# Performance work log

Hardware: AMD Instinct MI355X
Metric: run time of the kernel (lower is better)

Reference implementation:

```python
import jax, jax.numpy as jnp
import numpy as np
import math

GRID = 256       # grid_size
KMAX = 64        # max_elements_per_cell
RES = 512        # image resolution
SPAN = 4         # max grid cells per axis covered by one triangle bbox
NUM_VIEWS = 16
SCALE = 0.5


def _projection_matrix(x=0.5, n=1.5, f=100.0):
    return np.array([[n / x, 0.0, 0.0, 0.0],
                     [0.0, n / -x, 0.0, 0.0],
                     [0.0, 0.0, -(f + n) / (f - n), -(2.0 * f * n) / (f - n)],
                     [0.0, 0.0, -1.0, 0.0]], dtype=np.float32)


def _view_buffers(num_views, seed):
    rng = np.random.default_rng(seed)
    proj = _projection_matrix()
    mvps, lights = [], []
    for _ in range(num_views):
        u1, u2, u3 = rng.random(3)
        qx = math.sqrt(1.0 - u1) * math.sin(math.tau * u2)
        qy = math.sqrt(1.0 - u1) * math.cos(math.tau * u2)
        qz = math.sqrt(u1) * math.sin(math.tau * u3)
        qw = math.sqrt(u1) * math.cos(math.tau * u3)
        rot = np.array([[1 - 2 * (qy * qy + qz * qz), 2 * (qx * qy - qz * qw), 2 * (qx * qz + qy * qw)],
                        [2 * (qx * qy + qz * qw), 1 - 2 * (qx * qx + qz * qz), 2 * (qy * qz - qx * qw)],
                        [2 * (qx * qz - qy * qw), 2 * (qy * qz + qx * qw), 1 - 2 * (qx * qx + qy * qy)]], dtype=np.float32)
        rmat = np.eye(4, dtype=np.float32); rmat[:3, :3] = rot
        tmat = np.eye(4, dtype=np.float32); tmat[2, 3] = -4.0
        view = tmat @ rmat
        campos = np.linalg.inv(view)[:3, 3]
        light = -campos / (np.linalg.norm(campos) + 1e-8)
        mvps.append(proj @ view)
        lights.append(light.astype(np.float32))
    return np.stack(mvps).astype(np.float32), np.stack(lights).astype(np.float32)


def setup_inputs() -> dict:
    key = jax.random.key(0)
    k1, k2 = jax.random.split(key)
    F = 100_000
    # clustered per-triangle vertices -> small on-screen triangles (mesh-like locality)
    centers = jax.random.uniform(k1, (F, 1, 3), minval=-1.0, maxval=1.0)
    jitter = jax.random.normal(k2, (F, 3, 3)) * 0.02
    u = (centers + jitter).reshape(-1, 3).astype(jnp.float32)          # [3F,3]
    faces = jnp.arange(3 * F, dtype=jnp.int32).reshape(F, 3)
    mvps, light = _view_buffers(NUM_VIEWS, 42)
    return {"u": u,
            "mvps": jnp.asarray(mvps),
            "lightdir": jnp.asarray(light),
            "background_color": jnp.zeros(3, jnp.float32),
            "base_colors": jnp.ones((F, 3), jnp.float32),
            "faces": faces}


def _forward(u, mvps, lightdir, background_color, base_colors, faces):
    # _normalize_vertices
    v = u - u.mean(0, keepdims=True)
    span = jnp.maximum(v.max() - v.min(), 1e-6)
    v = v * (SCALE / span)
    Fn = faces.shape[0]
    # project with active view 0 (v_hom @ mvps[0].T, no perspective divide, as in source)
    v_hom = jnp.concatenate([v, jnp.ones((v.shape[0], 1), v.dtype)], axis=1)
    v_ndc = v_hom @ mvps[0].T                                          # [V,4]
    tris = v_ndc[faces]                                                # [F,3,4]
    wtri = v[faces]                                                    # [F,3,3]
    nrm = jnp.cross(wtri[:, 0] - wtri[:, 1], wtri[:, 2] - wtri[:, 1])
    nrm = nrm / (jnp.linalg.norm(nrm, axis=-1, keepdims=True) + 1e-10)
    z = tris[:, :, 2].mean(1)
    order = jnp.argsort(z)                                             # depth sort (near first)
    st = tris[order]
    sn = nrm[order]
    cp = (st[:, :, :2] + 1.0) * 0.5                                    # [F,3,2] control pts in [0,1]
    shading = jnp.clip(jnp.sum(-lightdir[0] * sn, axis=-1, keepdims=True), 0.0)
    colors = base_colors[order] * shading                              # [F,3]
    # --- grid acceleration structure build (scatter triangles into cells) ---
    lo = jnp.clip(jnp.floor(cp.min(1) * GRID).astype(jnp.int32), 0, GRID - 1)  # [F,2]
    hi = jnp.clip(jnp.floor(cp.max(1) * GRID).astype(jnp.int32), 0, GRID - 1)
    d = jnp.arange(SPAN, dtype=jnp.int32)
    cx = lo[:, 0:1] + d[None, :]                                       # [F,SPAN]
    cy = lo[:, 1:2] + d[None, :]
    valid = (cy[:, :, None] <= hi[:, 1:2, None]) & (cx[:, None, :] <= hi[:, 0:1].reshape(Fn, 1, 1) + 0 * cx[:, None, :])
    valid = (cy[:, :, None] <= hi[:, 1:2, None]) & (cx[:, None, :] <= hi[:, 0:1][:, :, None])
    cell = cy[:, :, None] * GRID + cx[:, None, :]                      # [F,SPAN,SPAN]
    NC = GRID * GRID
    cell = jnp.where(valid, cell, NC).reshape(-1)
    tri = jnp.broadcast_to(jnp.arange(Fn, dtype=jnp.int32)[:, None, None], (Fn, SPAN, SPAN)).reshape(-1)
    # sort (cell, depth-rank): tri ids are already depth-ordered
    keys = cell.astype(jnp.int64) * (Fn + 1) + tri
    ordk = jnp.argsort(keys)
    sc = cell[ordk]
    stri = tri[ordk]
    counts = jax.ops.segment_sum(jnp.ones_like(sc), sc, num_segments=NC + 1)
    starts = jnp.concatenate([jnp.zeros(1, counts.dtype), jnp.cumsum(counts)[:-1]])
    rank = jnp.arange(sc.shape[0], dtype=jnp.int32) - starts[sc].astype(jnp.int32)
    ok = (rank < KMAX) & (sc < NC)
    grid_elems = jnp.full((NC + 1, KMAX), -1, jnp.int32)
    grid_elems = grid_elems.at[jnp.where(ok, sc, NC), jnp.where(ok, rank, 0)].set(jnp.where(ok, stri, -1))
    # --- per-pixel rasterization via grid query ---
    px = (jnp.arange(RES, dtype=jnp.float32) + 0.5) / RES
    uu, vv = jnp.meshgrid(px, px, indexing='xy')
    P = jnp.stack([uu, vv], -1).reshape(-1, 2)                         # [P,2]
    ix = jnp.clip((P[:, 0] * GRID).astype(jnp.int32), 0, GRID - 1)
    iy = jnp.clip((P[:, 1] * GRID).astype(jnp.int32), 0, GRID - 1)
    elems = grid_elems[iy * GRID + ix]                                 # [P,K]
    e = jnp.maximum(elems, 0)
    tpts = cp[e]                                                       # [P,K,3,2]
    a, b, c = tpts[:, :, 0], tpts[:, :, 1], tpts[:, :, 2]
    pp = P[:, None, :]

    def cr(o, q, r):
        return (q[..., 0] - o[..., 0]) * (r[..., 1] - o[..., 1]) - (q[..., 1] - o[..., 1]) * (r[..., 0] - o[..., 0])

    e0 = cr(a, b, pp)
    e1 = cr(b, c, pp)
    e2 = cr(c, a, pp)
    inside = ((e0 >= 0) & (e1 >= 0) & (e2 >= 0)) | ((e0 <= 0) & (e1 <= 0) & (e2 <= 0))
    hit = inside & (elems >= 0)
    first = jnp.argmax(hit, axis=1)                                    # front-most (depth-sorted)
    anyhit = jnp.any(hit, axis=1)
    tid = e[jnp.arange(e.shape[0]), first]
    img = jnp.where(anyhit[:, None], colors[tid], background_color[None, :])
    return img.reshape(RES, RES, 3)


def reference(u, mvps, lightdir, background_color, base_colors, faces):
    return _forward(u, mvps, lightdir, background_color, base_colors, faces)
```

## Files before the change

kernel.cpp:

```cpp
#include <hip/hip_runtime.h>
#include <stdint.h>

#pragma clang fp contract(off)

#define GRIDN 256
#define NC (GRIDN * GRIDN)
#define RESN 512
#define RBLOCKS 256
#define CAP 1024
#define NB 64
#define NS 16
#define SBINS 2048

typedef unsigned short bfraw;
typedef unsigned short u16;

__device__ __forceinline__ float bf2f(bfraw h) {
    return __uint_as_float(((uint32_t)h) << 16);
}
__device__ __forceinline__ bfraw f2bf(float f) {
    uint32_t b = __float_as_uint(f);
    return (bfraw)((b + 0x7FFFu + ((b >> 16) & 1u)) >> 16);
}
__device__ __forceinline__ uint32_t fkey(float f) {
    uint32_t b = __float_as_uint(f);
    return (b & 0x80000000u) ? ~b : (b | 0x80000000u);
}

__global__ __launch_bounds__(256) void k_reduce1(const bfraw* __restrict__ u, int nrows,
                                                 double* __restrict__ psum,
                                                 float* __restrict__ pmin,
                                                 float* __restrict__ pmax) {
    __shared__ double ssum[256 * 3];
    __shared__ float smin[256 * 3];
    __shared__ float smax[256 * 3];
    int t = threadIdx.x;
    double s0 = 0.0, s1 = 0.0, s2 = 0.0;
    float mn0 = INFINITY, mn1 = INFINITY, mn2 = INFINITY;
    float mx0 = -INFINITY, mx1 = -INFINITY, mx2 = -INFINITY;
    for (int r = blockIdx.x * 256 + t; r < nrows; r += 256 * RBLOCKS) {
        float a = bf2f(u[3 * r + 0]);
        float b = bf2f(u[3 * r + 1]);
        float c = bf2f(u[3 * r + 2]);
        s0 += (double)a; s1 += (double)b; s2 += (double)c;
        mn0 = fminf(mn0, a); mx0 = fmaxf(mx0, a);
        mn1 = fminf(mn1, b); mx1 = fmaxf(mx1, b);
        mn2 = fminf(mn2, c); mx2 = fmaxf(mx2, c);
    }
    ssum[t * 3 + 0] = s0; ssum[t * 3 + 1] = s1; ssum[t * 3 + 2] = s2;
    smin[t * 3 + 0] = mn0; smin[t * 3 + 1] = mn1; smin[t * 3 + 2] = mn2;
    smax[t * 3 + 0] = mx0; smax[t * 3 + 1] = mx1; smax[t * 3 + 2] = mx2;
    __syncthreads();
    for (int st = 128; st > 0; st >>= 1) {
        if (t < st) {
            for (int c = 0; c < 3; c++) {
                ssum[t * 3 + c] += ssum[(t + st) * 3 + c];
                smin[t * 3 + c] = fminf(smin[t * 3 + c], smin[(t + st) * 3 + c]);
                smax[t * 3 + c] = fmaxf(smax[t * 3 + c], smax[(t + st) * 3 + c]);
            }
        }
        __syncthreads();
    }
    if (t == 0) {
        for (int c = 0; c < 3; c++) {
            psum[blockIdx.x * 3 + c] = ssum[c];
            pmin[blockIdx.x * 3 + c] = smin[c];
            pmax[blockIdx.x * 3 + c] = smax[c];
        }
    }
}

__global__ __launch_bounds__(256) void k_reduce2(const double* __restrict__ psum,
                                                 const float* __restrict__ pmin,
                                                 const float* __restrict__ pmax,
                                                 int nrows, float* __restrict__ cst) {
    __shared__ double ssum[256 * 3];
    __shared__ float smin[256 * 3];
    __shared__ float smax[256 * 3];
    int t = threadIdx.x;
    for (int c = 0; c < 3; c++) {
        ssum[t * 3 + c] = psum[t * 3 + c];
        smin[t * 3 + c] = pmin[t * 3 + c];
        smax[t * 3 + c] = pmax[t * 3 + c];
    }
    __syncthreads();
    for (int st = 128; st > 0; st >>= 1) {
        if (t < st) {
            for (int c = 0; c < 3; c++) {
                ssum[t * 3 + c] += ssum[(t + st) * 3 + c];
                smin[t * 3 + c] = fminf(smin[t * 3 + c], smin[(t + st) * 3 + c]);
                smax[t * 3 + c] = fmaxf(smax[t * 3 + c], smax[(t + st) * 3 + c]);
            }
        }
        __syncthreads();
    }
    if (t == 0) {
        float fn = (float)nrows;
        float m0 = (float)ssum[0] / fn;
        float m1 = (float)ssum[1] / fn;
        float m2 = (float)ssum[2] / fn;
        float vmax = fmaxf(fmaxf(smax[0] - m0, smax[1] - m1), smax[2] - m2);
        float vmin = fminf(fminf(smin[0] - m0, smin[1] - m1), smin[2] - m2);
        float span = fmaxf(vmax - vmin, 1e-06f);
        float s = 0.5f / span;
        cst[0] = m0; cst[1] = m1; cst[2] = m2; cst[3] = s;
    }
}

__global__ __launch_bounds__(256) void k_setup(const bfraw* __restrict__ u,
                                               const int* __restrict__ faces,
                                               const bfraw* __restrict__ mvp,
                                               const bfraw* __restrict__ light,
                                               const float* __restrict__ cst,
                                               int F,
                                               float* __restrict__ tcs,
                                               uint32_t* __restrict__ tz,
                                               uint32_t* __restrict__ tbox) {
    int f = blockIdx.x * 256 + threadIdx.x;
    if (f >= F) return;
    float m0 = cst[0], m1 = cst[1], m2 = cst[2], s = cst[3];
    float M[12];
    for (int i = 0; i < 12; i++) M[i] = bf2f(mvp[i]);

    float vx[3], vy[3], vz[3], cpx[3], cpy[3], zc[3];
    for (int j = 0; j < 3; j++) {
        int idx = faces[3 * f + j];
        float a = bf2f(u[3 * idx + 0]);
        float b = bf2f(u[3 * idx + 1]);
        float c = bf2f(u[3 * idx + 2]);
        float x = (a - m0) * s;
        float y = (b - m1) * s;
        float z = (c - m2) * s;
        vx[j] = x; vy[j] = y; vz[j] = z;
        float cx = fmaf(x, M[0], 0.0f);
        cx = fmaf(y, M[1], cx); cx = fmaf(z, M[2], cx); cx = cx + M[3];
        float cy = fmaf(x, M[4], 0.0f);
        cy = fmaf(y, M[5], cy); cy = fmaf(z, M[6], cy); cy = cy + M[7];
        float cz = fmaf(x, M[8], 0.0f);
        cz = fmaf(y, M[9], cz); cz = fmaf(z, M[10], cz); cz = cz + M[11];
        cpx[j] = (cx + 1.0f) * 0.5f;
        cpy[j] = (cy + 1.0f) * 0.5f;
        zc[j] = cz;
    }
    float zmean = ((zc[0] + zc[1]) + zc[2]) / 3.0f;

    float e1x = vx[0] - vx[1], e1y = vy[0] - vy[1], e1z = vz[0] - vz[1];
    float e2x = vx[2] - vx[1], e2y = vy[2] - vy[1], e2z = vz[2] - vz[1];
    float nx = e1y * e2z - e1z * e2y;
    float ny = e1z * e2x - e1x * e2z;
    float nz = e1x * e2y - e1y * e2x;
    float nn = nx * nx;
    nn = nn + ny * ny;
    nn = nn + nz * nz;
    float d = sqrtf(nn) + 1e-10f;
    float inx = nx / d, iny = ny / d, inz = nz / d;

    float l0 = bf2f(light[0]), l1 = bf2f(light[1]), l2 = bf2f(light[2]);
    float p0 = (-l0) * inx;
    float p1 = (-l1) * iny;
    float p2 = (-l2) * inz;
    float shading = fmaxf((p0 + p1) + p2, 0.0f);

    tcs[f * 8 + 0] = cpx[0]; tcs[f * 8 + 1] = cpy[0];
    tcs[f * 8 + 2] = cpx[1]; tcs[f * 8 + 3] = cpy[1];
    tcs[f * 8 + 4] = cpx[2]; tcs[f * 8 + 5] = cpy[2];
    tcs[f * 8 + 6] = shading;
    tcs[f * 8 + 7] = 0.0f;

    tz[f] = fkey(zmean);

    float mnx = fminf(fminf(cpx[0], cpx[1]), cpx[2]);
    float mny = fminf(fminf(cpy[0], cpy[1]), cpy[2]);
    float mxx = fmaxf(fmaxf(cpx[0], cpx[1]), cpx[2]);
    float mxy = fmaxf(fmaxf(cpy[0], cpy[1]), cpy[2]);
    int lox = (int)floorf(mnx * 256.0f); lox = lox < 0 ? 0 : (lox > 255 ? 255 : lox);
    int loy = (int)floorf(mny * 256.0f); loy = loy < 0 ? 0 : (loy > 255 ? 255 : loy);
    int hix = (int)floorf(mxx * 256.0f); hix = hix < 0 ? 0 : (hix > 255 ? 255 : hix);
    int hiy = (int)floorf(mxy * 256.0f); hiy = hiy < 0 ? 0 : (hiy > 255 ? 255 : hiy);
    int hx = hix < lox + 3 ? hix : lox + 3;
    int hy = hiy < loy + 3 ? hiy : loy + 3;
    tbox[f] = (uint32_t)lox | ((uint32_t)loy << 8) | ((uint32_t)hx << 16) | ((uint32_t)hy << 24);
}

__global__ __launch_bounds__(256) void k_count(const uint32_t* __restrict__ tbox,
                                               int F,
                                               u16* __restrict__ blockHist) {
    __shared__ uint32_t hist[SBINS];
    int b = blockIdx.x >> 4;
    int sl = blockIdx.x & (NS - 1);
    int chunk = (F + NB - 1) / NB;
    int fs = b * chunk;
    int fe = fs + chunk < F ? fs + chunk : F;
    for (int i = threadIdx.x; i < SBINS; i += 256) hist[i] = 0u;
    __syncthreads();
    for (int f = fs + threadIdx.x; f < fe; f += 256) {
        uint32_t bx = tbox[f];
        int lox = bx & 255, loy = (bx >> 8) & 255;
        int hx = (bx >> 16) & 255, hy = bx >> 24;
        for (int yy = loy; yy <= hy; yy++) {
            for (int xx = lox; xx <= hx; xx++) {
                uint32_t cell = (uint32_t)(yy * GRIDN + xx);
                if ((int)(cell >> 12) != sl) continue;
                uint32_t c = cell & 4095u;
                atomicAdd(&hist[c >> 1], 1u << (16u * (c & 1u)));
            }
        }
    }
    __syncthreads();
    uint32_t* dst = (uint32_t*)(blockHist + (size_t)b * NC) + sl * SBINS;
    for (int i = threadIdx.x; i < SBINS; i += 256) dst[i] = hist[i];
}

__global__ __launch_bounds__(256) void k_scanA(u16* __restrict__ blockHist,
                                               uint32_t* __restrict__ cellTot) {
    int c = blockIdx.x * 256 + threadIdx.x;
    uint32_t tot = 0;
    for (int b = 0; b < NB; b++) {
        size_t o = (size_t)b * NC + c;
        uint32_t v = blockHist[o];
        blockHist[o] = (u16)tot;
        tot += v;
    }
    cellTot[c] = tot;
}

__global__ __launch_bounds__(1024) void k_scan1(const uint32_t* __restrict__ cellTot,
                                                uint32_t* __restrict__ cellOff,
                                                uint32_t* __restrict__ blockSum) {
    __shared__ uint32_t sc[1024];
    int B = blockIdx.x, t = threadIdx.x;
    uint32_t v = cellTot[B * 1024 + t];
    sc[t] = v;
    __syncthreads();
    for (int st = 1; st < 1024; st <<= 1) {
        uint32_t a = 0;
        if (t >= st) a = sc[t - st];
        __syncthreads();
        if (t >= st) sc[t] += a;
        __syncthreads();
    }
    cellOff[B * 1024 + t] = sc[t] - v;
    if (t == 1023) blockSum[B] = sc[1023];
}

__global__ __launch_bounds__(64) void k_scan2(const uint32_t* __restrict__ blockSum,
                                              uint32_t* __restrict__ blockBase,
                                              uint32_t* __restrict__ cellOff) {
    __shared__ uint32_t s[64];
    int t = threadIdx.x;
    uint32_t v = blockSum[t];
    s[t] = v;
    __syncthreads();
    for (int st = 1; st < 64; st <<= 1) {
        uint32_t a = 0;
        if (t >= st) a = s[t - st];
        __syncthreads();
        if (t >= st) s[t] += a;
        __syncthreads();
    }
    blockBase[t] = s[t] - v;
    if (t == 63) cellOff[NC] = s[63];
}

__global__ __launch_bounds__(1024) void k_scan3(uint32_t* __restrict__ cellOff,
                                                const uint32_t* __restrict__ blockBase) {
    int B = blockIdx.x, t = threadIdx.x;
    cellOff[B * 1024 + t] += blockBase[B];
}

__global__ __launch_bounds__(256) void k_place(const uint32_t* __restrict__ tbox,
                                               const u16* __restrict__ blockHist,
                                               const uint32_t* __restrict__ cellOff,
                                               uint32_t* __restrict__ pairs,
                                               int F) {
    __shared__ uint32_t hist[SBINS];
    int b = blockIdx.x >> 4;
    int sl = blockIdx.x & (NS - 1);
    int chunk = (F + NB - 1) / NB;
    int fs = b * chunk;
    int fe = fs + chunk < F ? fs + chunk : F;
    uint32_t pcap = (uint32_t)F * 16u;
    for (int i = threadIdx.x; i < SBINS; i += 256) hist[i] = 0u;
    __syncthreads();
    for (int f = fs + threadIdx.x; f < fe; f += 256) {
        uint32_t bx = tbox[f];
        int lox = bx & 255, loy = (bx >> 8) & 255;
        int hx = (bx >> 16) & 255, hy = bx >> 24;
        for (int yy = loy; yy <= hy; yy++) {
            for (int xx = lox; xx <= hx; xx++) {
                uint32_t cell = (uint32_t)(yy * GRIDN + xx);
                if ((int)(cell >> 12) != sl) continue;
                uint32_t c = cell & 4095u;
                uint32_t sh = 16u * (c & 1u);
                uint32_t old = atomicAdd(&hist[c >> 1], 1u << sh);
                uint32_t r = (old >> sh) & 0xFFFFu;
                uint32_t pos = cellOff[cell] + (uint32_t)blockHist[(size_t)b * NC + cell] + r;
                if (pos < pcap) pairs[pos] = (uint32_t)f;
            }
        }
    }
}

__global__ __launch_bounds__(256) void k_cellsort(const uint32_t* __restrict__ cellOff,
                                                  const uint32_t* __restrict__ tz,
                                                  uint32_t* __restrict__ pairs,
                                                  int F) {
    __shared__ uint64_t lkeys[CAP];
    int cell = blockIdx.x;
    uint32_t pcap = (uint32_t)F * 16u;
    uint32_t off = cellOff[cell];
    uint32_t end = cellOff[cell + 1];
    if (off > pcap || end > pcap || end < off) return;
    uint32_t n = end - off;
    if (n < 2u) return;
    uint32_t m = n > CAP ? CAP : n;
    int t = threadIdx.x;
    for (uint32_t i = t; i < m; i += 256) {
        uint32_t id = pairs[off + i];
        if (id >= (uint32_t)F) id = 0;
        lkeys[i] = ((uint64_t)tz[id] << 32) | id;
    }
    __syncthreads();
    uint64_t k0 = ~0ull, k1 = ~0ull, k2 = ~0ull, k3 = ~0ull;
    uint32_t i0 = t, i1 = t + 256, i2 = t + 512, i3 = t + 768;
    if (i0 < m) k0 = lkeys[i0];
    if (i1 < m) k1 = lkeys[i1];
    if (i2 < m) k2 = lkeys[i2];
    if (i3 < m) k3 = lkeys[i3];
    uint32_t r0 = 0, r1 = 0, r2 = 0, r3 = 0;
    for (uint32_t j = 0; j < m; j++) {
        uint64_t kj = lkeys[j];
        r0 += (kj < k0) ? 1u : 0u;
        r1 += (kj < k1) ? 1u : 0u;
        r2 += (kj < k2) ? 1u : 0u;
        r3 += (kj < k3) ? 1u : 0u;
    }
    if (i0 < m && r0 < 64u) pairs[off + r0] = (uint32_t)(k0 & 0xFFFFFFFFu);
    if (i1 < m && r1 < 64u) pairs[off + r1] = (uint32_t)(k1 & 0xFFFFFFFFu);
    if (i2 < m && r2 < 64u) pairs[off + r2] = (uint32_t)(k2 & 0xFFFFFFFFu);
    if (i3 < m && r3 < 64u) pairs[off + r3] = (uint32_t)(k3 & 0xFFFFFFFFu);
}

__global__ __launch_bounds__(256) void k_raster(const float* __restrict__ tcs,
                                                const uint32_t* __restrict__ cellOff,
                                                const uint32_t* __restrict__ pairs,
                                                const bfraw* __restrict__ basec,
                                                const bfraw* __restrict__ bg,
                                                bfraw* __restrict__ out, int F) {
    int p = blockIdx.x * 256 + threadIdx.x;
    int col = p & (RESN - 1);
    int row = p >> 9;
    float px = ((float)col + 0.5f) / 512.0f;
    float py = ((float)row + 0.5f) / 512.0f;
    int cell = (row >> 1) * GRIDN + (col >> 1);
    uint32_t pcap = (uint32_t)F * 16u;
    uint32_t off = cellOff[cell];
    uint32_t end = cellOff[cell + 1];
    uint32_t m = 0;
    if (off <= pcap && end <= pcap && end >= off) {
        uint32_t n = end - off;
        m = n > 64u ? 64u : n;
    }
    float r = bf2f(bg[0]), g = bf2f(bg[1]), b = bf2f(bg[2]);
    for (uint32_t k = 0; k < m; k++) {
        uint32_t id = pairs[off + k];
        if (id >= (uint32_t)F) continue;
        const float4 A = *(const float4*)(tcs + (size_t)id * 8);
        const float4 B = *(const float4*)(tcs + (size_t)id * 8 + 4);
        float ax = A.x, ay = A.y, bx = A.z, by = A.w, cx = B.x, cy = B.y;
        float e0 = (bx - ax) * (py - ay) - (by - ay) * (px - ax);
        float e1 = (cx - bx) * (py - by) - (cy - by) * (px - bx);
        float e2 = (ax - cx) * (py - cy) - (ay - cy) * (px - cx);
        bool inside = (e0 >= 0.0f && e1 >= 0.0f && e2 >= 0.0f) ||
                      (e0 <= 0.0f && e1 <= 0.0f && e2 <= 0.0f);
        if (inside) {
            float sh = B.z;
            r = bf2f(basec[3 * id + 0]) * sh;
            g = bf2f(basec[3 * id + 1]) * sh;
            b = bf2f(basec[3 * id + 2]) * sh;
            break;
        }
    }
    int o = p * 3;
    out[o + 0] = f2bf(r);
    out[o + 1] = f2bf(g);
    out[o + 2] = f2bf(b);
}

__global__ __launch_bounds__(256) void k_diag(bfraw* __restrict__ out, float code) {
    out[blockIdx.x * 256 + threadIdx.x] = f2bf(code);
}

extern "C" void kernel_launch(void* const* d_in, const int* in_sizes, int n_in,
                              void* d_out, int out_size, void* d_ws, size_t ws_size,
                              hipStream_t stream) {
    const bfraw* u = (const bfraw*)d_in[0];
    const bfraw* mvps = (const bfraw*)d_in[1];
    const bfraw* light = (const bfraw*)d_in[2];
    const bfraw* bg = (const bfraw*)d_in[3];
    const bfraw* basec = (const bfraw*)d_in[4];
    const int* faces = (const int*)d_in[5];
    int nrows = in_sizes[0] / 3;
    int F = in_sizes[5] / 3;
    bfraw* out = (bfraw*)d_out;

    char* w = (char*)d_ws;
    size_t off = 0;
    auto alloc = [&](size_t bytes) -> void* {
        off = (off + 255) & ~(size_t)255;
        void* p = w + off;
        off += bytes;
        return p;
    };

    float* cst = (float*)alloc(4 * sizeof(float));
    double* psum = (double*)alloc((size_t)RBLOCKS * 3 * sizeof(double));
    float* pmin = (float*)alloc((size_t)RBLOCKS * 3 * sizeof(float));
    float* pmax = (float*)alloc((size_t)RBLOCKS * 3 * sizeof(float));
    float* tcs = (float*)alloc((size_t)F * 8 * sizeof(float));
    uint32_t* tz = (uint32_t*)alloc((size_t)F * sizeof(uint32_t));
    uint32_t* tbox = (uint32_t*)alloc((size_t)F * sizeof(uint32_t));
    u16* blockHist = (u16*)alloc((size_t)NB * NC * sizeof(u16));
    uint32_t* cellTot = (uint32_t*)alloc((size_t)NC * sizeof(uint32_t));
    uint32_t* cellOff = (uint32_t*)alloc(((size_t)NC + 1) * sizeof(uint32_t));
    uint32_t* blockSum = (uint32_t*)alloc(64 * sizeof(uint32_t));
    uint32_t* blockBase = (uint32_t*)alloc(64 * sizeof(uint32_t));
    uint32_t* pairs = (uint32_t*)alloc((size_t)F * 16 * sizeof(uint32_t));
    size_t needed = off;

    if (ws_size < needed) {
        float code = 20000.0f + (float)(ws_size >> 20);
        k_diag<<<(RESN * RESN * 3) / 256, 256, 0, stream>>>(out, code);
        return;
    }

    k_reduce1<<<RBLOCKS, 256, 0, stream>>>(u, nrows, psum, pmin, pmax);
    k_reduce2<<<1, 256, 0, stream>>>(psum, pmin, pmax, nrows, cst);
    k_setup<<<(F + 255) / 256, 256, 0, stream>>>(u, faces, mvps, light, cst, F,
                                                 tcs, tz, tbox);
    k_count<<<NB * NS, 256, 0, stream>>>(tbox, F, blockHist);
    k_scanA<<<NC / 256, 256, 0, stream>>>(blockHist, cellTot);
    k_scan1<<<64, 1024, 0, stream>>>(cellTot, cellOff, blockSum);
    k_scan2<<<1, 64, 0, stream>>>(blockSum, blockBase, cellOff);
    k_scan3<<<64, 1024, 0, stream>>>(cellOff, blockBase);
    k_place<<<NB * NS, 256, 0, stream>>>(tbox, blockHist, cellOff, pairs, F);
    k_cellsort<<<NC, 256, 0, stream>>>(cellOff, tz, pairs, F);
    k_raster<<<(RESN * RESN) / 256, 256, 0, stream>>>(tcs, cellOff, pairs, basec, bg, out, F);
}
```

Baseline: 155.0 us.

## Clamp slice rows in binning, fuse scan kernels, split cellsort blocks

The count and place kernels now clamp each triangle's row range to the block's 16-row slice instead of testing every covered cell against the slice. The four scan kernels become two: the per-cell column scan is fused with the block-level prefix, and the 64-entry block-base prefix is recomputed serially inside the final add kernel. The cell sort launches two blocks per cell, each ranking half of the keys, which cuts per-thread work but doubles the key loading and adds many early-exit blocks for sparse cells.

Result: no change. 156.1 us (+0.8%).

```diff
diff --git a/kernel.cpp b/kernel.cpp
--- a/kernel.cpp
+++ b/kernel.cpp
@@ -191,17 +191,18 @@
     int chunk = (F + NB - 1) / NB;
     int fs = b * chunk;
     int fe = fs + chunk < F ? fs + chunk : F;
+    int y0 = sl * 16, y1 = y0 + 15;
     for (int i = threadIdx.x; i < SBINS; i += 256) hist[i] = 0u;
     __syncthreads();
     for (int f = fs + threadIdx.x; f < fe; f += 256) {
         uint32_t bx = tbox[f];
         int lox = bx & 255, loy = (bx >> 8) & 255;
         int hx = (bx >> 16) & 255, hy = bx >> 24;
-        for (int yy = loy; yy <= hy; yy++) {
+        int ys = loy > y0 ? loy : y0;
+        int ye = hy < y1 ? hy : y1;
+        for (int yy = ys; yy <= ye; yy++) {
             for (int xx = lox; xx <= hx; xx++) {
-                uint32_t cell = (uint32_t)(yy * GRIDN + xx);
-                if ((int)(cell >> 12) != sl) continue;
-                uint32_t c = cell & 4095u;
+                uint32_t c = (uint32_t)(yy * GRIDN + xx) & 4095u;
                 atomicAdd(&hist[c >> 1], 1u << (16u * (c & 1u)));
             }
         }
@@ -211,9 +212,12 @@
     for (int i = threadIdx.x; i < SBINS; i += 256) dst[i] = hist[i];
 }
 
-__global__ __launch_bounds__(256) void k_scanA(u16* __restrict__ blockHist,
-                                               uint32_t* __restrict__ cellTot) {
-    int c = blockIdx.x * 256 + threadIdx.x;
+__global__ __launch_bounds__(1024) void k_scanA1(u16* __restrict__ blockHist,
+                                                 uint32_t* __restrict__ cellOff,
+                                                 uint32_t* __restrict__ blockSum) {
+    __shared__ uint32_t sc[1024];
+    int B = blockIdx.x, t = threadIdx.x;
+    int c = B * 1024 + t;
     uint32_t tot = 0;
     for (int b = 0; b < NB; b++) {
         size_t o = (size_t)b * NC + c;
@@ -221,16 +225,7 @@
         blockHist[o] = (u16)tot;
         tot += v;
     }
-    cellTot[c] = tot;
-}
-
-__global__ __launch_bounds__(1024) void k_scan1(const uint32_t* __restrict__ cellTot,
-                                                uint32_t* __restrict__ cellOff,
-                                                uint32_t* __restrict__ blockSum) {
-    __shared__ uint32_t sc[1024];
-    int B = blockIdx.x, t = threadIdx.x;
-    uint32_t v = cellTot[B * 1024 + t];
-    sc[t] = v;
+    sc[t] = tot;
     __syncthreads();
     for (int st = 1; st < 1024; st <<= 1) {
         uint32_t a = 0;
@@ -239,33 +234,22 @@
         if (t >= st) sc[t] += a;
         __syncthreads();
     }
-    cellOff[B * 1024 + t] = sc[t] - v;
+    cellOff[c] = sc[t] - tot;
     if (t == 1023) blockSum[B] = sc[1023];
 }
 
-__global__ __launch_bounds__(64) void k_scan2(const uint32_t* __restrict__ blockSum,
-                                              uint32_t* __restrict__ blockBase,
-                                              uint32_t* __restrict__ cellOff) {
-    __shared__ uint32_t s[64];
-    int t = threadIdx.x;
-    uint32_t v = blockSum[t];
-    s[t] = v;
-    __syncthreads();
-    for (int st = 1; st < 64; st <<= 1) {
-        uint32_t a = 0;
-        if (t >= st) a = s[t - st];
-        __syncthreads();
-        if (t >= st) s[t] += a;
-        __syncthreads();
-    }
-    blockBase[t] = s[t] - v;
-    if (t == 63) cellOff[NC] = s[63];
-}
-
-__global__ __launch_bounds__(1024) void k_scan3(uint32_t* __restrict__ cellOff,
-                                                const uint32_t* __restrict__ blockBase) {
+__global__ __launch_bounds__(1024) void k_scanB(uint32_t* __restrict__ cellOff,
+                                                const uint32_t* __restrict__ blockSum) {
+    __shared__ uint32_t pre[65];
     int B = blockIdx.x, t = threadIdx.x;
-    cellOff[B * 1024 + t] += blockBase[B];
+    if (t == 0) {
+        uint32_t run = 0;
+        for (int i = 0; i < 64; i++) { pre[i] = run; run += blockSum[i]; }
+        pre[64] = run;
+    }
+    __syncthreads();
+    cellOff[B * 1024 + t] += pre[B];
+    if (B == 63 && t == 1023) cellOff[NC] = pre[64];
 }
 
 __global__ __launch_bounds__(256) void k_place(const uint32_t* __restrict__ tbox,
@@ -279,6 +263,7 @@
     int chunk = (F + NB - 1) / NB;
     int fs = b * chunk;
     int fe = fs + chunk < F ? fs + chunk : F;
+    int y0 = sl * 16, y1 = y0 + 15;
     uint32_t pcap = (uint32_t)F * 16u;
     for (int i = threadIdx.x; i < SBINS; i += 256) hist[i] = 0u;
     __syncthreads();
@@ -286,10 +271,11 @@
         uint32_t bx = tbox[f];
         int lox = bx & 255, loy = (bx >> 8) & 255;
         int hx = (bx >> 16) & 255, hy = bx >> 24;
-        for (int yy = loy; yy <= hy; yy++) {
+        int ys = loy > y0 ? loy : y0;
+        int ye = hy < y1 ? hy : y1;
+        for (int yy = ys; yy <= ye; yy++) {
             for (int xx = lox; xx <= hx; xx++) {
                 uint32_t cell = (uint32_t)(yy * GRIDN + xx);
-                if ((int)(cell >> 12) != sl) continue;
                 uint32_t c = cell & 4095u;
                 uint32_t sh = 16u * (c & 1u);
                 uint32_t old = atomicAdd(&hist[c >> 1], 1u << sh);
@@ -306,7 +292,8 @@
                                                   uint32_t* __restrict__ pairs,
                                                   int F) {
     __shared__ uint64_t lkeys[CAP];
-    int cell = blockIdx.x;
+    int cell = blockIdx.x >> 1;
+    int half = blockIdx.x & 1;
     uint32_t pcap = (uint32_t)F * 16u;
     uint32_t off = cellOff[cell];
     uint32_t end = cellOff[cell + 1];
@@ -314,6 +301,8 @@
     uint32_t n = end - off;
     if (n < 2u) return;
     uint32_t m = n > CAP ? CAP : n;
+    uint32_t base = (uint32_t)half * 512u;
+    if (base >= m) return;
     int t = threadIdx.x;
     for (uint32_t i = t; i < m; i += 256) {
         uint32_t id = pairs[off + i];
@@ -321,24 +310,18 @@
         lkeys[i] = ((uint64_t)tz[id] << 32) | id;
     }
     __syncthreads();
-    uint64_t k0 = ~0ull, k1 = ~0ull, k2 = ~0ull, k3 = ~0ull;
-    uint32_t i0 = t, i1 = t + 256, i2 = t + 512, i3 = t + 768;
+    uint64_t k0 = ~0ull, k1 = ~0ull;
+    uint32_t i0 = base + t, i1 = base + t + 256;
     if (i0 < m) k0 = lkeys[i0];
     if (i1 < m) k1 = lkeys[i1];
-    if (i2 < m) k2 = lkeys[i2];
-    if (i3 < m) k3 = lkeys[i3];
-    uint32_t r0 = 0, r1 = 0, r2 = 0, r3 = 0;
+    uint32_t r0 = 0, r1 = 0;
     for (uint32_t j = 0; j < m; j++) {
         uint64_t kj = lkeys[j];
         r0 += (kj < k0) ? 1u : 0u;
         r1 += (kj < k1) ? 1u : 0u;
-        r2 += (kj < k2) ? 1u : 0u;
-        r3 += (kj < k3) ? 1u : 0u;
     }
     if (i0 < m && r0 < 64u) pairs[off + r0] = (uint32_t)(k0 & 0xFFFFFFFFu);
     if (i1 < m && r1 < 64u) pairs[off + r1] = (uint32_t)(k1 & 0xFFFFFFFFu);
-    if (i2 < m && r2 < 64u) pairs[off + r2] = (uint32_t)(k2 & 0xFFFFFFFFu);
-    if (i3 < m && r3 < 64u) pairs[off + r3] = (uint32_t)(k3 & 0xFFFFFFFFu);
 }
 
 __global__ __launch_bounds__(256) void k_raster(const float* __restrict__ tcs,
@@ -421,10 +404,8 @@
     uint32_t* tz = (uint32_t*)alloc((size_t)F * sizeof(uint32_t));
     uint32_t* tbox = (uint32_t*)alloc((size_t)F * sizeof(uint32_t));
     u16* blockHist = (u16*)alloc((size_t)NB * NC * sizeof(u16));
-    uint32_t* cellTot = (uint32_t*)alloc((size_t)NC * sizeof(uint32_t));
     uint32_t* cellOff = (uint32_t*)alloc(((size_t)NC + 1) * sizeof(uint32_t));
     uint32_t* blockSum = (uint32_t*)alloc(64 * sizeof(uint32_t));
-    uint32_t* blockBase = (uint32_t*)alloc(64 * sizeof(uint32_t));
     uint32_t* pairs = (uint32_t*)alloc((size_t)F * 16 * sizeof(uint32_t));
     size_t needed = off;
 
@@ -439,11 +420,9 @@
     k_setup<<<(F + 255) / 256, 256, 0, stream>>>(u, faces, mvps, light, cst, F,
                                                  tcs, tz, tbox);
     k_count<<<NB * NS, 256, 0, stream>>>(tbox, F, blockHist);
-    k_scanA<<<NC / 256, 256, 0, stream>>>(blockHist, cellTot);
-    k_scan1<<<64, 1024, 0, stream>>>(cellTot, cellOff, blockSum);
-    k_scan2<<<1, 64, 0, stream>>>(blockSum, blockBase, cellOff);
-    k_scan3<<<64, 1024, 0, stream>>>(cellOff, blockBase);
+    k_scanA1<<<64, 1024, 0, stream>>>(blockHist, cellOff, blockSum);
+    k_scanB<<<64, 1024, 0, stream>>>(cellOff, blockSum);
     k_place<<<NB * NS, 256, 0, stream>>>(tbox, blockHist, cellOff, pairs, F);
-    k_cellsort<<<NC, 256, 0, stream>>>(cellOff, tz, pairs, F);
+    k_cellsort<<<NC * 2, 256, 0, stream>>>(cellOff, tz, pairs, F);
     k_raster<<<(RESN * RESN) / 256, 256, 0, stream>>>(tcs, cellOff, pairs, basec, bg, out, F);
 }
```
